# Kernel tuning notes

Hardware: AMD Instinct MI355X
Metric: run time of the kernel (lower is better)

Reference implementation:

```python
import jax, jax.numpy as jnp
import numpy as np

NUM_RADIAL = 16
HIDDEN = 128
CUTOFF = 5.0
N_NODES = 20000
N_EDGES = 320000


def bessel_rbf(d):
    # DimeNet-style Bessel radial basis: sqrt(2/c) * sin(n*pi*d/c) / d, n=1..NUM_RADIAL
    n = jnp.arange(1, NUM_RADIAL + 1, dtype=d.dtype)  # [R]
    freq = n * (np.pi / CUTOFF)
    norm = np.sqrt(2.0 / CUTOFF)
    return norm * jnp.sin(d[:, None] * freq[None, :]) / d[:, None]  # [E, R]


def setup_inputs() -> dict:
    key = jax.random.key(0)
    k = jax.random.split(key, 8)
    node_embs = jax.random.normal(k[0], (N_NODES, HIDDEN), dtype=jnp.float32)
    edge_index = jax.random.randint(k[1], (2, N_EDGES), 0, N_NODES, dtype=jnp.int32)
    # distances in (0.5, CUTOFF) to avoid division blowup near 0
    edge_weight = 0.5 + (CUTOFF - 0.5) * jax.random.uniform(k[2], (N_EDGES,), dtype=jnp.float32)
    s0 = 1.0 / np.sqrt(NUM_RADIAL)
    s1 = 1.0 / np.sqrt(3 * HIDDEN)
    W_rbf0 = jax.random.uniform(k[3], (NUM_RADIAL, HIDDEN), jnp.float32, -s0, s0)
    b_rbf0 = jax.random.uniform(k[4], (HIDDEN,), jnp.float32, -s0, s0)
    W_lin = jax.random.uniform(k[5], (3 * HIDDEN, HIDDEN), jnp.float32, -s1, s1)
    b_lin = jax.random.uniform(k[6], (HIDDEN,), jnp.float32, -s1, s1)
    W_rbf1 = jax.random.normal(k[7], (NUM_RADIAL, HIDDEN), jnp.float32) * np.sqrt(2.0 / (NUM_RADIAL + HIDDEN))
    return {"node_embs": node_embs, "edge_index": edge_index, "edge_weight": edge_weight,
            "W_rbf0": W_rbf0, "b_rbf0": b_rbf0, "W_lin": W_lin, "b_lin": b_lin, "W_rbf1": W_rbf1}


def reference(node_embs, edge_index, edge_weight, W_rbf0, b_rbf0, W_lin, b_lin, W_rbf1):
    rbf = bessel_rbf(edge_weight)                              # [E, R]
    rbf0 = jax.nn.silu(rbf @ W_rbf0 + b_rbf0)                  # [E, H]
    src = node_embs[edge_index[0]]                             # [E, H] gather
    dst = node_embs[edge_index[1]]                             # [E, H] gather
    h = jnp.concatenate([src, dst, rbf0], axis=-1)             # [E, 3H]
    e1 = jax.nn.silu(h @ W_lin + b_lin)                        # [E, H]
    e2 = (rbf @ W_rbf1) * e1                                   # [E, H]
    return (e1, e2)
```

## Files before the change

kernel.cpp:

```cpp
#include <hip/hip_runtime.h>

#define E_EDGES 320000
#define N_NODES 20000
#define HID 128
#define K3 384
#define NR 16
#define RS 24
#define NT 1024
#define D0f 0.5f
#define DRANGE 4.5f
#define NS 136
#define PBLK 313
#define TBLK (NT / 32)

#define P_BYTES (N_NODES * 256 * 2)
#define T_OFF   P_BYTES
#define WS_NEED (T_OFF + NT * 256 * 2)

typedef float f32x16 __attribute__((ext_vector_type(16)));
typedef float f32x4  __attribute__((ext_vector_type(4)));
typedef short short8 __attribute__((ext_vector_type(8)));
typedef unsigned short u16x4 __attribute__((ext_vector_type(4)));
typedef _Float16 f16x4 __attribute__((ext_vector_type(4)));

__device__ __forceinline__ unsigned short f2bf(float x) {
  union { float f; unsigned u; } v; v.f = x;
  unsigned u = v.u + 0x7fffu + ((v.u >> 16) & 1u);
  return (unsigned short)(u >> 16);
}
__device__ __forceinline__ float bf2f(unsigned short b) {
  union { unsigned u; float f; } v; v.u = ((unsigned)b) << 16;
  return v.f;
}
__device__ __forceinline__ unsigned pk2(float a, float b) {
  union { float f; unsigned u; } va, vb; va.f = a; vb.f = b;
  unsigned ua = va.u + 0x7fffu + ((va.u >> 16) & 1u);
  unsigned ub = vb.u + 0x7fffu + ((vb.u >> 16) & 1u);
  return (ua >> 16) | (ub & 0xffff0000u);
}

#define BAR() asm volatile("s_waitcnt lgkmcnt(0)\n\ts_barrier" ::: "memory")

__global__ __launch_bounds__(512)
void prep_fused(const float* __restrict__ ne, const float* __restrict__ Wlin,
                const float* __restrict__ W0, const float* __restrict__ b0,
                const float* __restrict__ blin, const float* __restrict__ W1,
                unsigned short* __restrict__ P, _Float16* __restrict__ T)
{
  __shared__ __align__(16) unsigned short WtL[256 * NS];
  __shared__ __align__(16) unsigned short ndL[64 * NS];
  __shared__ float rbf0L[32][128];
  __shared__ float rbfL[32][16];

  const int t = threadIdx.x;

  if (blockIdx.x < PBLK) {
    const int lane = t & 63, w = t >> 6;
    const int er = w >> 2, cc = w & 3;
    const int l31 = lane & 31, hi = lane >> 5, koff = hi * 8;
    const int n0 = blockIdx.x * 64;

    #pragma unroll
    for (int rep = 0; rep < 4; ++rep) {
      int idx = rep * 512 + t;
      int kp = idx >> 5, c4 = idx & 31;
      float4 a = ((const float4*)Wlin)[(2 * kp) * 32 + c4];
      float4 b = ((const float4*)Wlin)[(2 * kp + 1) * 32 + c4];
      *(unsigned*)&WtL[(4 * c4 + 0) * NS + 2 * kp] = pk2(a.x, b.x);
      *(unsigned*)&WtL[(4 * c4 + 1) * NS + 2 * kp] = pk2(a.y, b.y);
      *(unsigned*)&WtL[(4 * c4 + 2) * NS + 2 * kp] = pk2(a.z, b.z);
      *(unsigned*)&WtL[(4 * c4 + 3) * NS + 2 * kp] = pk2(a.w, b.w);
    }
    #pragma unroll
    for (int rep = 0; rep < 4; ++rep) {
      int idx = rep * 512 + t;
      int kp = idx >> 5, c4 = idx & 31;
      float4 a = ((const float4*)Wlin)[4096 + (2 * kp) * 32 + c4];
      float4 b = ((const float4*)Wlin)[4096 + (2 * kp + 1) * 32 + c4];
      *(unsigned*)&WtL[(128 + 4 * c4 + 0) * NS + 2 * kp] = pk2(a.x, b.x);
      *(unsigned*)&WtL[(128 + 4 * c4 + 1) * NS + 2 * kp] = pk2(a.y, b.y);
      *(unsigned*)&WtL[(128 + 4 * c4 + 2) * NS + 2 * kp] = pk2(a.z, b.z);
      *(unsigned*)&WtL[(128 + 4 * c4 + 3) * NS + 2 * kp] = pk2(a.w, b.w);
    }
    #pragma unroll
    for (int rep = 0; rep < 4; ++rep) {
      int idx = rep * 512 + t;
      int r = idx >> 5, q = idx & 31;
      int n = n0 + r; if (n > N_NODES - 1) n = N_NODES - 1;
      float4 v = ((const float4*)ne)[n * 32 + q];
      uint2 pv; pv.x = pk2(v.x, v.y); pv.y = pk2(v.z, v.w);
      *(uint2*)&ndL[r * NS + q * 4] = pv;
    }
    BAR();

    const int arow = er * 32 + l31;
    #pragma unroll
    for (int cg = 0; cg < 2; ++cg) {
      int bcol2 = cg * 128 + cc * 32 + l31;
      f32x16 acc = {0,0,0,0,0,0,0,0,0,0,0,0,0,0,0,0};
      #pragma unroll
      for (int ks = 0; ks < 8; ++ks) {
        short8 a = *(const short8*)&ndL[arow * NS + ks * 16 + koff];
        short8 b = *(const short8*)&WtL[bcol2 * NS + ks * 16 + koff];
        acc = __builtin_amdgcn_mfma_f32_32x32x16_bf16(a, b, acc, 0, 0, 0);
      }
      #pragma unroll
      for (int i = 0; i < 16; ++i) {
        int row = (i & 3) + 8 * (i >> 2) + 4 * hi;
        int n = n0 + er * 32 + row;
        if (n < N_NODES) P[n * 256 + bcol2] = f2bf(acc[i]);
      }
    }
  } else {
    const int gp0 = (blockIdx.x - PBLK) * 32;

    {
      int gp = t >> 4, r = t & 15;
      float d = D0f + (float)(gp0 + gp) * (DRANGE / (float)(NT - 1));
      rbfL[gp][r] = 0.63245553f * __sinf(d * (float)(r + 1) * 0.62831853f) / d;
    }
    __syncthreads();
    for (int it = t; it < 32 * 128; it += 512) {
      int gp = it >> 7, j = it & 127;
      float u = b0[j];
      #pragma unroll
      for (int r = 0; r < NR; ++r) u += rbfL[gp][r] * W0[r * HID + j];
      rbf0L[gp][j] = u / (1.f + __expf(-u));
    }
    __syncthreads();

    const int c = t & 127, qd = t >> 7;
    float q[8], s[8];
    #pragma unroll
    for (int k = 0; k < 8; ++k) { q[k] = blin[c]; s[k] = 0.f; }
    for (int j = 0; j < HID; ++j) {
      float wv = Wlin[(256 + j) * HID + c];
      #pragma unroll
      for (int k = 0; k < 8; ++k) q[k] += rbf0L[qd * 8 + k][j] * wv;
    }
    #pragma unroll
    for (int r = 0; r < NR; ++r) {
      float wv = W1[r * HID + c];
      #pragma unroll
      for (int k = 0; k < 8; ++k) s[k] += rbfL[qd * 8 + k][r] * wv;
    }
    #pragma unroll
    for (int k = 0; k < 8; ++k) {
      int g = gp0 + qd * 8 + k;
      T[g * 256 + c]       = (_Float16)q[k];
      T[g * 256 + 128 + c] = (_Float16)s[k];
    }
  }
}

__global__ __launch_bounds__(256)
void edge_main(const int* __restrict__ eidx, const float* __restrict__ ew,
               const unsigned short* __restrict__ P, const _Float16* __restrict__ T,
               float* __restrict__ out)
{
  const int g  = blockIdx.x * 256 + threadIdx.x;
  const int e  = g >> 5;
  const int c4 = (g & 31) << 2;

  const int sn = eidx[e];
  const int dn = eidx[E_EDGES + e];
  const float d = ew[e];

  float tt = (d - D0f) * ((float)(NT - 1) / DRANGE);
  int i0 = (int)tt;
  if (i0 < 0) i0 = 0;
  if (i0 > NT - 2) i0 = NT - 2;
  const float fr = tt - (float)i0;

  const _Float16* T0 = &T[i0 * 256];
  const f16x4 q0 = *(const f16x4*)&T0[c4];
  const f16x4 q1 = *(const f16x4*)&T0[256 + c4];
  const f16x4 s0 = *(const f16x4*)&T0[128 + c4];
  const f16x4 s1 = *(const f16x4*)&T0[256 + 128 + c4];
  const u16x4 pa = *(const u16x4*)&P[sn * 256 + c4];
  const u16x4 pb = *(const u16x4*)&P[dn * 256 + 128 + c4];

  f32x4 E1, E2;
  #pragma unroll
  for (int j = 0; j < 4; ++j) {
    float q = (float)q0[j] + fr * ((float)q1[j] - (float)q0[j]);
    float s = (float)s0[j] + fr * ((float)s1[j] - (float)s0[j]);
    float x = bf2f(pa[j]) + bf2f(pb[j]) + q;
    float v = x * __fdividef(1.f, 1.f + __expf(-x));
    E1[j] = v;
    E2[j] = s * v;
  }

  const long gi = (long)e * HID + c4;
  __builtin_nontemporal_store(E1, (f32x4*)&out[gi]);
  __builtin_nontemporal_store(E2, (f32x4*)&out[(long)E_EDGES * HID + gi]);
}

#define HS 392
__global__ __launch_bounds__(512, 2)
void edge_feat_kernel_fb(const float* __restrict__ node_embs,
                         const int* __restrict__ eidx,
                         const float* __restrict__ ew,
                         const float* __restrict__ Wrbf0,
                         const float* __restrict__ brbf0,
                         const float* __restrict__ Wlin,
                         const float* __restrict__ blin,
                         const float* __restrict__ Wrbf1,
                         float* __restrict__ out)
{
  __shared__ __align__(16) unsigned short hT[2][64 * HS];
  __shared__ __align__(16) unsigned short rbfb2[2][64 * RS];

  const int t = threadIdx.x, lane = t & 63, w = t >> 6;
  const int er = w >> 2, cc = w & 3;
  const int l31 = lane & 31, hi = lane >> 5, koff = hi * 8;
  const int arow = er * 32 + l31, bcol = cc * 32 + l31;
  const float bl = blin[bcol], b0 = brbf0[bcol];

  {
    unsigned short* WtL = &hT[0][0];
    for (int i = t; i < K3 * HID; i += 512) {
      int k = i >> 7, col = i & 127;
      WtL[col * HS + k] = f2bf(Wlin[i]);
    }
    BAR();
  }
  short8 wb[24];
  #pragma unroll
  for (int ks = 0; ks < 24; ++ks)
    wb[ks] = *(const short8*)&hT[0][bcol * HS + ks * 16 + koff];
  asm volatile("s_waitcnt lgkmcnt(0)" ::: "memory");
  __builtin_amdgcn_s_barrier();

  short8 w0f, w1f;
  #pragma unroll
  for (int j = 0; j < 8; ++j) {
    w0f[j] = (short)f2bf(Wrbf0[(koff + j) * HID + bcol]);
    w1f[j] = (short)f2bf(Wrbf1[(koff + j) * HID + bcol]);
  }

  int tile = blockIdx.x;
  {
    #pragma unroll
    for (int rep = 0; rep < 8; ++rep) {
      int idx = rep * 512 + t;
      int which = idx >> 11, r2 = idx & 2047;
      int e_loc = r2 >> 5, q = r2 & 31;
      int node = eidx[which * E_EDGES + tile * 64 + e_loc];
      const float4 v = ((const float4*)node_embs)[node * 32 + q];
      uint2 pv; pv.x = pk2(v.x, v.y); pv.y = pk2(v.z, v.w);
      *(uint2*)&hT[0][e_loc * HS + which * 128 + q * 4] = pv;
    }
    #pragma unroll
    for (int rep = 0; rep < 2; ++rep) {
      int i = rep * 512 + t;
      int e_loc = i >> 4, r = i & 15;
      float d = ew[tile * 64 + e_loc];
      float v = 0.63245553f * __sinf(d * (float)(r + 1) * 0.62831853f) / d;
      rbfb2[0][e_loc * RS + r] = f2bf(v);
    }
  }
  BAR();

  int cur = 0;
  for (; tile < E_EDGES / 64; tile += (int)gridDim.x) {
    const int nt = tile + (int)gridDim.x;
    const bool hasnext = (nt < E_EDGES / 64);
    const int e0 = tile * 64;

    float4 g4[8]; float dv[2];
    if (hasnext) {
      #pragma unroll
      for (int rep = 0; rep < 8; ++rep) {
        int idx = rep * 512 + t;
        int which = idx >> 11, r2 = idx & 2047;
        int e_loc = r2 >> 5, q = r2 & 31;
        int node = eidx[which * E_EDGES + nt * 64 + e_loc];
        g4[rep] = ((const float4*)node_embs)[node * 32 + q];
      }
      #pragma unroll
      for (int rep = 0; rep < 2; ++rep)
        dv[rep] = ew[nt * 64 + ((rep * 512 + t) >> 4)];
    }

    f32x16 r0 = {0,0,0,0,0,0,0,0,0,0,0,0,0,0,0,0};
    f32x16 sacc = {0,0,0,0,0,0,0,0,0,0,0,0,0,0,0,0};
    short8 ra = *(const short8*)&rbfb2[cur][arow * RS + koff];
    r0   = __builtin_amdgcn_mfma_f32_32x32x16_bf16(ra, w0f, r0, 0, 0, 0);
    sacc = __builtin_amdgcn_mfma_f32_32x32x16_bf16(ra, w1f, sacc, 0, 0, 0);
    #pragma unroll
    for (int i = 0; i < 16; ++i) {
      int row = (i & 3) + 8 * (i >> 2) + 4 * hi;
      float x = r0[i] + b0;
      float s = x / (1.f + __expf(-x));
      hT[cur][(er * 32 + row) * HS + 256 + bcol] = f2bf(s);
    }
    BAR();

    f32x16 acc = {0,0,0,0,0,0,0,0,0,0,0,0,0,0,0,0};
    #pragma unroll
    for (int ks = 0; ks < 24; ++ks) {
      short8 a = *(const short8*)&hT[cur][arow * HS + ks * 16 + koff];
      acc = __builtin_amdgcn_mfma_f32_32x32x16_bf16(a, wb[ks], acc, 0, 0, 0);
    }

    if (hasnext) {
      #pragma unroll
      for (int rep = 0; rep < 2; ++rep) {
        int i = rep * 512 + t;
        int e_loc = i >> 4, r = i & 15;
        float d = dv[rep];
        float v = 0.63245553f * __sinf(d * (float)(r + 1) * 0.62831853f) / d;
        rbfb2[cur ^ 1][e_loc * RS + r] = f2bf(v);
      }
      #pragma unroll
      for (int rep = 0; rep < 8; ++rep) {
        int idx = rep * 512 + t;
        int which = idx >> 11, r2 = idx & 2047;
        int e_loc = r2 >> 5, q = r2 & 31;
        uint2 pv; pv.x = pk2(g4[rep].x, g4[rep].y); pv.y = pk2(g4[rep].z, g4[rep].w);
        *(uint2*)&hT[cur ^ 1][e_loc * HS + which * 128 + q * 4] = pv;
      }
    }

    #pragma unroll
    for (int i = 0; i < 16; ++i) {
      int row = (i & 3) + 8 * (i >> 2) + 4 * hi;
      int e_loc = er * 32 + row;
      float x = acc[i] + bl;
      float e1 = x / (1.f + __expf(-x));
      float e2 = sacc[i] * e1;
      long gi = (long)(e0 + e_loc) * HID + bcol;
      __builtin_nontemporal_store(e1, &out[gi]);
      __builtin_nontemporal_store(e2, &out[(long)E_EDGES * HID + gi]);
    }
    BAR();
    cur ^= 1;
  }
}

extern "C" void kernel_launch(void* const* d_in, const int* in_sizes, int n_in,
                              void* d_out, int out_size, void* d_ws, size_t ws_size,
                              hipStream_t stream) {
  const float* node_embs = (const float*)d_in[0];
  const int*   eidx      = (const int*)d_in[1];
  const float* ew        = (const float*)d_in[2];
  const float* Wrbf0     = (const float*)d_in[3];
  const float* brbf0     = (const float*)d_in[4];
  const float* Wlin      = (const float*)d_in[5];
  const float* blin      = (const float*)d_in[6];
  const float* Wrbf1     = (const float*)d_in[7];
  float* out = (float*)d_out;

  if (ws_size >= (size_t)WS_NEED) {
    char* ws = (char*)d_ws;
    unsigned short* P = (unsigned short*)ws;
    _Float16* T       = (_Float16*)(ws + T_OFF);

    prep_fused<<<PBLK + TBLK, 512, 0, stream>>>(node_embs, Wlin, Wrbf0, brbf0,
                                                blin, Wrbf1, P, T);
    edge_main<<<E_EDGES * 32 / 256, 256, 0, stream>>>(eidx, ew, P, T, out);
  } else {
    edge_feat_kernel_fb<<<256, 512, 0, stream>>>(node_embs, eidx, ew, Wrbf0, brbf0,
                                                 Wlin, blin, Wrbf1, out);
  }
}
```

Measured before the change: 93.61 us.

## Persist edge_main threads with prefetched edge indices and interleaved T table

Interleaves the q and s halves of the distance lookup table so each thread reads one 16-byte vector per table row instead of two 8-byte loads. The edge kernel becomes a grid-stride loop of 1250 blocks of 512 threads, each handling 16 edges, and prefetches the next edge's indices and distance while computing the current one. This aims to cut launch and wave overhead and hide index-load latency, at the cost of fewer resident waves to hide gather latency.

```diff
diff --git a/kernel.cpp b/kernel.cpp
--- a/kernel.cpp
+++ b/kernel.cpp
@@ -12,6 +12,8 @@
 #define NS 136
 #define PBLK 313
 #define TBLK (NT / 32)
+#define NTHREADS 640000
+#define EM_ITERS 16
 
 #define P_BYTES (N_NODES * 256 * 2)
 #define T_OFF   P_BYTES
@@ -21,7 +23,7 @@
 typedef float f32x4  __attribute__((ext_vector_type(4)));
 typedef short short8 __attribute__((ext_vector_type(8)));
 typedef unsigned short u16x4 __attribute__((ext_vector_type(4)));
-typedef _Float16 f16x4 __attribute__((ext_vector_type(4)));
+typedef _Float16 f16x8 __attribute__((ext_vector_type(8)));
 
 __device__ __forceinline__ unsigned short f2bf(float x) {
   union { float f; unsigned u; } v; v.f = x;
@@ -130,6 +132,7 @@
     __syncthreads();
 
     const int c = t & 127, qd = t >> 7;
+    const int cb = c >> 2, cr = c & 3;
     float q[8], s[8];
     #pragma unroll
     for (int k = 0; k < 8; ++k) { q[k] = blin[c]; s[k] = 0.f; }
@@ -147,53 +150,65 @@
     #pragma unroll
     for (int k = 0; k < 8; ++k) {
       int g = gp0 + qd * 8 + k;
-      T[g * 256 + c]       = (_Float16)q[k];
-      T[g * 256 + 128 + c] = (_Float16)s[k];
-    }
-  }
-}
-
-__global__ __launch_bounds__(256)
+      T[g * 256 + cb * 8 + cr]     = (_Float16)q[k];
+      T[g * 256 + cb * 8 + 4 + cr] = (_Float16)s[k];
+    }
+  }
+}
+
+__global__ __launch_bounds__(512)
 void edge_main(const int* __restrict__ eidx, const float* __restrict__ ew,
                const unsigned short* __restrict__ P, const _Float16* __restrict__ T,
                float* __restrict__ out)
 {
-  const int g  = blockIdx.x * 256 + threadIdx.x;
-  const int e  = g >> 5;
-  const int c4 = (g & 31) << 2;
-
-  const int sn = eidx[e];
-  const int dn = eidx[E_EDGES + e];
-  const float d = ew[e];
-
-  float tt = (d - D0f) * ((float)(NT - 1) / DRANGE);
-  int i0 = (int)tt;
-  if (i0 < 0) i0 = 0;
-  if (i0 > NT - 2) i0 = NT - 2;
-  const float fr = tt - (float)i0;
-
-  const _Float16* T0 = &T[i0 * 256];
-  const f16x4 q0 = *(const f16x4*)&T0[c4];
-  const f16x4 q1 = *(const f16x4*)&T0[256 + c4];
-  const f16x4 s0 = *(const f16x4*)&T0[128 + c4];
-  const f16x4 s1 = *(const f16x4*)&T0[256 + 128 + c4];
-  const u16x4 pa = *(const u16x4*)&P[sn * 256 + c4];
-  const u16x4 pb = *(const u16x4*)&P[dn * 256 + 128 + c4];
-
-  f32x4 E1, E2;
-  #pragma unroll
-  for (int j = 0; j < 4; ++j) {
-    float q = (float)q0[j] + fr * ((float)q1[j] - (float)q0[j]);
-    float s = (float)s0[j] + fr * ((float)s1[j] - (float)s0[j]);
-    float x = bf2f(pa[j]) + bf2f(pb[j]) + q;
-    float v = x * __fdividef(1.f, 1.f + __expf(-x));
-    E1[j] = v;
-    E2[j] = s * v;
-  }
-
-  const long gi = (long)e * HID + c4;
-  __builtin_nontemporal_store(E1, (f32x4*)&out[gi]);
-  __builtin_nontemporal_store(E2, (f32x4*)&out[(long)E_EDGES * HID + gi]);
+  const int tid = blockIdx.x * 512 + threadIdx.x;
+  const int c4  = (tid & 31) << 2;
+  const int tb8 = c4 << 1;
+
+  int g = tid;
+  int e = g >> 5;
+  int sn = eidx[e];
+  int dn = eidx[E_EDGES + e];
+  float d = ew[e];
+
+  #pragma unroll 1
+  for (int it = 0; it < EM_ITERS; ++it) {
+    int sn2, dn2; float d2; int en = 0;
+    if (it < EM_ITERS - 1) {
+      en  = (g + NTHREADS) >> 5;
+      sn2 = eidx[en];
+      dn2 = eidx[E_EDGES + en];
+      d2  = ew[en];
+    }
+
+    float tt = (d - D0f) * ((float)(NT - 1) / DRANGE);
+    int i0 = (int)tt;
+    if (i0 < 0) i0 = 0;
+    if (i0 > NT - 2) i0 = NT - 2;
+    const float fr = tt - (float)i0;
+
+    const f16x8 r0 = *(const f16x8*)&T[i0 * 256 + tb8];
+    const f16x8 r1 = *(const f16x8*)&T[(i0 + 1) * 256 + tb8];
+    const u16x4 pa = *(const u16x4*)&P[sn * 256 + c4];
+    const u16x4 pb = *(const u16x4*)&P[dn * 256 + 128 + c4];
+
+    f32x4 E1, E2;
+    #pragma unroll
+    for (int j = 0; j < 4; ++j) {
+      float q = (float)r0[j] + fr * ((float)r1[j] - (float)r0[j]);
+      float s = (float)r0[4 + j] + fr * ((float)r1[4 + j] - (float)r0[4 + j]);
+      float x = bf2f(pa[j]) + bf2f(pb[j]) + q;
+      float v = x * __fdividef(1.f, 1.f + __expf(-x));
+      E1[j] = v;
+      E2[j] = s * v;
+    }
+
+    const long gi = (long)e * HID + c4;
+    __builtin_nontemporal_store(E1, (f32x4*)&out[gi]);
+    __builtin_nontemporal_store(E2, (f32x4*)&out[(long)E_EDGES * HID + gi]);
+
+    g += NTHREADS; e = en; sn = sn2; dn = dn2; d = d2;
+  }
 }
 
 #define HS 392
@@ -359,7 +374,7 @@
 
     prep_fused<<<PBLK + TBLK, 512, 0, stream>>>(node_embs, Wlin, Wrbf0, brbf0,
                                                 blin, Wrbf1, P, T);
-    edge_main<<<E_EDGES * 32 / 256, 256, 0, stream>>>(eidx, ew, P, T, out);
+    edge_main<<<NTHREADS / 512, 512, 0, stream>>>(eidx, ew, P, T, out);
   } else {
     edge_feat_kernel_fb<<<256, 512, 0, stream>>>(node_embs, eidx, ew, Wrbf0, brbf0,
                                                  Wlin, blin, Wrbf1, out);
```

Result: slower. 96.32 us (+2.9%).
